# Kernel tuning notes

Measured on AMD Instinct MI355X. Metric: run time of the kernel, lower is better.

Reference implementation:

```python
import jax, jax.numpy as jnp
import numpy as np

D_MODEL = 1024
H = 16
D_K = D_MODEL // H
NEG = -1e9


def setup_inputs() -> dict:
    key = jax.random.key(0)
    ks = jax.random.split(key, 13)
    B, S = 4, 2048
    q = jax.random.normal(ks[0], (B, S, D_MODEL), dtype=jnp.float32)
    k = jax.random.normal(ks[1], (B, S, D_MODEL), dtype=jnp.float32)
    v = jax.random.normal(ks[2], (B, S, D_MODEL), dtype=jnp.float32)
    mask = jax.random.randint(ks[3], (B, 1, S, S), 0, 2, dtype=jnp.int32)
    s = 1.0 / np.sqrt(D_MODEL)
    wq = jax.random.uniform(ks[4], (D_MODEL, D_MODEL), jnp.float32, -s, s)
    bq = jax.random.uniform(ks[5], (D_MODEL,), jnp.float32, -s, s)
    wk = jax.random.uniform(ks[6], (D_MODEL, D_MODEL), jnp.float32, -s, s)
    bk = jax.random.uniform(ks[7], (D_MODEL,), jnp.float32, -s, s)
    wv = jax.random.uniform(ks[8], (D_MODEL, D_MODEL), jnp.float32, -s, s)
    bv = jax.random.uniform(ks[9], (D_MODEL,), jnp.float32, -s, s)
    wo = jax.random.uniform(ks[10], (D_MODEL, D_MODEL), jnp.float32, -s, s)
    bo = jax.random.uniform(ks[11], (D_MODEL,), jnp.float32, -s, s)
    return {"q": q, "k": k, "v": v, "mask": mask,
            "wq": wq, "bq": bq, "wk": wk, "bk": bk,
            "wv": wv, "bv": bv, "wo": wo, "bo": bo}


def reference(q, k, v, mask, wq, bq, wk, bk, wv, bv, wo, bo):
    B, S, _ = q.shape
    # projections (torch Linear: x @ W.T + b)
    query = q @ wq.T + bq
    key_ = k @ wk.T + bk
    value = v @ wv.T + bv
    # [B, S, H, D_K] -> [B, H, S, D_K]
    query = query.reshape(B, S, H, D_K).transpose(0, 2, 1, 3)
    key_ = key_.reshape(B, S, H, D_K).transpose(0, 2, 1, 3)
    value = value.reshape(B, S, H, D_K).transpose(0, 2, 1, 3)
    scores = jnp.einsum('bhqd,bhkd->bhqk', query, key_) / jnp.sqrt(jnp.float32(D_K))
    scores = jnp.where(mask == 0, jnp.float32(NEG), scores)
    attn = jax.nn.softmax(scores, axis=-1)  # dropout p=0 -> identity
    x = jnp.einsum('bhqk,bhkd->bhqd', attn, value)
    x = x.transpose(0, 2, 1, 3).reshape(B, S, D_MODEL)
    return x @ wo.T + bo
```

## Files before the change

kernel.cpp:

```cpp
#include <hip/hip_runtime.h>
#include <stdint.h>
#include <stddef.h>


typedef unsigned short ushort_t;
typedef unsigned long long u64;
typedef __attribute__((ext_vector_type(8))) short short8;
typedef __attribute__((ext_vector_type(4))) float floatx4;
typedef __attribute__((ext_vector_type(4))) unsigned short ushort4v;
typedef __attribute__((ext_vector_type(4))) unsigned int uint4v;

#define QSCALE (0.125f * 1.4426950408889634f)

__device__ __forceinline__ ushort_t f2bf(float f) {
    union { float ff; unsigned int i; } v; v.ff = f;
    unsigned int u = v.i;
    return (ushort_t)((u + 0x7fffu + ((u >> 16) & 1u)) >> 16);
}
__device__ __forceinline__ unsigned int pk2(float a, float b) {
    unsigned int r;
    asm("v_cvt_pk_bf16_f32 %0, %1, %2" : "=v"(r) : "v"(a), "v"(b));
    return r;
}
__device__ __forceinline__ float fexp2(float x) {
#if __has_builtin(__builtin_amdgcn_exp2f)
    return __builtin_amdgcn_exp2f(x);
#else
    return exp2f(x);
#endif
}
__device__ __forceinline__ void g2l16(const void* g, void* l) {
    __builtin_amdgcn_global_load_lds(
        (const __attribute__((address_space(1))) void*)(uintptr_t)g,
        (__attribute__((address_space(3))) void*)(uint32_t)(uintptr_t)l,
        16, 0, 0);
}

__global__ __launch_bounds__(256) void prep(
    const float* __restrict__ wq, const float* __restrict__ wk,
    const float* __restrict__ wv, const float* __restrict__ wo,
    const float* __restrict__ q, const float* __restrict__ k,
    const float* __restrict__ v, const int* __restrict__ mask,
    ushort_t* __restrict__ Wb, ushort_t* __restrict__ Qb,
    ushort_t* __restrict__ Kb, ushort_t* __restrict__ Vb,
    u64* __restrict__ mbits)
{
    const int bx = blockIdx.x, tid = threadIdx.x;
    if (bx < 14336) {
        const float* src; ushort_t* dst; int idx;
        if (bx < 2048) {
            const int seg = bx >> 9;
            src = (seg == 0) ? wq : (seg == 1) ? wk : (seg == 2) ? wv : wo;
            dst = Wb + (size_t)seg * 1024 * 1024;
            idx = (bx & 511) * 256 + tid;
        } else {
            const int b2 = bx - 2048;
            const int z = b2 >> 12;
            src = (z == 0) ? q : (z == 1) ? k : v;
            dst = (z == 0) ? Qb : (z == 1) ? Kb : Vb;
            idx = (b2 & 4095) * 256 + tid;
        }
        const float4 f0 = ((const float4*)src)[idx * 2];
        const float4 f1 = ((const float4*)src)[idx * 2 + 1];
        uint4v c;
        c.x = pk2(f0.x, f0.y); c.y = pk2(f0.z, f0.w);
        c.z = pk2(f1.x, f1.y); c.w = pk2(f1.z, f1.w);
        ((uint4v*)dst)[idx] = c;
    } else {
        const int b3 = bx - 14336;
        const int base = b3 * 4096;
#pragma unroll
        for (int it = 0; it < 16; ++it) {
            const int gid = base + it * 256 + tid;
            const u64 bits = __ballot(mask[gid] != 0);
            if ((tid & 63) == 0) mbits[gid >> 6] = bits;
        }
    }
}

__device__ __forceinline__ void gemm_core(
    const ushort_t* __restrict__ Ain, const ushort_t* __restrict__ W,
    const float* __restrict__ bias, void* __restrict__ Cout,
    float scale, int mode)
{
    constexpr int N = 1024, K = 1024;
    __shared__ alignas(16) ushort_t As[4][128 * 32];
    __shared__ alignas(16) ushort_t Bs[2][128 * 32];

    const int tid  = threadIdx.x;
    const int lane = tid & 63;
    const int w    = tid >> 6;
    const int quad = lane >> 4;
    const int l16  = lane & 15;
    const int wm = w >> 1, wn = w & 1;
    const int bm = blockIdx.x * 128, bn = blockIdx.y * 128;

    const int ar0 = tid >> 2,         acs0 = ((tid & 3) ^ (ar0 & 3)) * 8;
    const int ar1 = (tid + 256) >> 2, acs1 = ((tid & 3) ^ (ar1 & 3)) * 8;
    const ushort_t* Ast0 = Ain + (size_t)(bm + ar0) * K + acs0;
    const ushort_t* Ast1 = Ain + (size_t)(bm + ar1) * K + acs1;
    const ushort_t* Wst0 = W + (size_t)(bn + ar0) * K + acs0;
    const ushort_t* Wst1 = W + (size_t)(bn + ar1) * K + acs1;

    const int ksw = (quad ^ (l16 & 3)) * 8;
    int asoff[4], bsoff[4];
#pragma unroll
    for (int i = 0; i < 4; i++) {
        asoff[i] = (wm * 64 + i * 16 + l16) * 32 + ksw;
        bsoff[i] = (wn * 64 + i * 16 + l16) * 32 + ksw;
    }

    floatx4 acc[4][4] = {};

    g2l16(Wst0,      &Bs[0][tid * 8]);
    g2l16(Wst1,      &Bs[0][(tid + 256) * 8]);
    __builtin_amdgcn_sched_barrier(0);
    g2l16(Ast0,      &As[0][tid * 8]);
    g2l16(Ast1,      &As[0][(tid + 256) * 8]);
    g2l16(Ast0 + 32, &As[1][tid * 8]);
    g2l16(Ast1 + 32, &As[1][(tid + 256) * 8]);
    g2l16(Ast0 + 64, &As[2][tid * 8]);
    g2l16(Ast1 + 64, &As[2][(tid + 256) * 8]);

#define GITER(AS, WS, NW, NA, KW, KA, DO_W, DO_A, TOPW) do {                  \
    asm volatile("s_waitcnt " TOPW);                                          \
    asm volatile("s_waitcnt lgkmcnt(0)");                                     \
    __builtin_amdgcn_sched_barrier(0);                                        \
    __builtin_amdgcn_s_barrier();                                             \
    __builtin_amdgcn_sched_barrier(0);                                        \
    if (DO_W) {                                                               \
        g2l16(Wst0 + (KW), &Bs[NW][tid * 8]);                                 \
        g2l16(Wst1 + (KW), &Bs[NW][(tid + 256) * 8]);                         \
    }                                                                         \
    __builtin_amdgcn_sched_barrier(0);                                        \
    if (DO_A) {                                                               \
        g2l16(Ast0 + (KA), &As[NA][tid * 8]);                                 \
        g2l16(Ast1 + (KA), &As[NA][(tid + 256) * 8]);                         \
    }                                                                         \
    __builtin_amdgcn_sched_barrier(0);                                        \
    {                                                                         \
        short8 af[4], bf[4];                                                  \
        _Pragma("unroll")                                                     \
        for (int i = 0; i < 4; i++) af[i] = *(const short8*)&As[AS][asoff[i]];\
        _Pragma("unroll")                                                     \
        for (int i = 0; i < 4; i++) bf[i] = *(const short8*)&Bs[WS][bsoff[i]];\
        _Pragma("unroll")                                                     \
        for (int mi = 0; mi < 4; mi++)                                        \
        _Pragma("unroll")                                                     \
        for (int ni = 0; ni < 4; ni++)                                        \
            acc[mi][ni] = __builtin_amdgcn_mfma_f32_16x16x32_bf16(            \
                af[mi], bf[ni], acc[mi][ni], 0, 0, 0);                        \
    }                                                                         \
} while (0)

    GITER(0, 0, 1, 3,  32,  96, true, true, "vmcnt(4)");
    GITER(1, 1, 0, 0,  64, 128, true, true, "vmcnt(2)");
    GITER(2, 0, 1, 1,  96, 160, true, true, "vmcnt(2)");
    GITER(3, 1, 0, 2, 128, 192, true, true, "vmcnt(2)");
    for (int j = 1; j < 7; ++j) {
        const int kb = j * 128;
        GITER(0, 0, 1, 3, kb + 32,  kb + 96,  true, true, "vmcnt(2)");
        GITER(1, 1, 0, 0, kb + 64,  kb + 128, true, true, "vmcnt(2)");
        GITER(2, 0, 1, 1, kb + 96,  kb + 160, true, true, "vmcnt(2)");
        GITER(3, 1, 0, 2, kb + 128, kb + 192, true, true, "vmcnt(2)");
    }
    GITER(0, 0, 1, 3, 928, 992, true,  true,  "vmcnt(2)");
    GITER(1, 1, 0, 0, 960, 0,   true,  false, "vmcnt(2)");
    GITER(2, 0, 1, 0, 992, 0,   true,  false, "vmcnt(0)");
    GITER(3, 1, 0, 0, 0,   0,   false, false, "vmcnt(0)");
#undef GITER

#pragma unroll
    for (int ni = 0; ni < 4; ni++) {
        const int n = bn + wn * 64 + ni * 16 + l16;
        const float bv_ = bias[n];
#pragma unroll
        for (int mi = 0; mi < 4; mi++) {
            const int mbase = bm + wm * 64 + mi * 16 + quad * 4;
            if (mode == 2) {
                const int b_ = mbase >> 11, s0 = mbase & 2047;
                const int h = n >> 6, d = n & 63;
                ushort4v pk_;
#pragma unroll
                for (int r = 0; r < 4; r++)
                    pk_[r] = f2bf((acc[mi][ni][r] + bv_) * scale);
                *(ushort4v*)&((ushort_t*)Cout)[
                    (((size_t)(b_ * 16 + h)) * 64 + d) * 2048 + s0] = pk_;
            } else {
#pragma unroll
                for (int r = 0; r < 4; r++) {
                    const int m = mbase + r;
                    const float of = (acc[mi][ni][r] + bv_) * scale;
                    if (mode == 0) {
                        ((float*)Cout)[(size_t)m * N + n] = of;
                    } else {
                        const int b_ = m >> 11, s = m & 2047;
                        const int h = n >> 6, d = n & 63;
                        ((ushort_t*)Cout)[(((size_t)(b_ * 16 + h)) * 2048 + s) * 64 + d]
                            = f2bf(of);
                    }
                }
            }
        }
    }
}

__global__ __launch_bounds__(256, 3) void gemm_qkv(
    const ushort_t* __restrict__ Qb, const ushort_t* __restrict__ Kb,
    const ushort_t* __restrict__ Vb, const ushort_t* __restrict__ Wb,
    const float* __restrict__ bq, const float* __restrict__ bk,
    const float* __restrict__ bv,
    ushort_t* __restrict__ Qp, ushort_t* __restrict__ Kp,
    ushort_t* __restrict__ Vtp)
{
    const int z = blockIdx.z;
    const ushort_t* A = (z == 0) ? Qb : (z == 1) ? Kb : Vb;
    const ushort_t* W = Wb + (size_t)z * 1024 * 1024;
    const float* bi = (z == 0) ? bq : (z == 1) ? bk : bv;
    void* C = (z == 0) ? (void*)Qp : (z == 1) ? (void*)Kp : (void*)Vtp;
    const float sc = (z == 0) ? QSCALE : 1.0f;
    const int mode = (z == 2) ? 2 : 1;
    gemm_core(A, W, bi, C, sc, mode);
}

__global__ __launch_bounds__(256, 3) void gemm_out(
    const ushort_t* __restrict__ X, const ushort_t* __restrict__ W,
    const float* __restrict__ bo, float* __restrict__ out)
{
    gemm_core(X, W, bo, out, 1.0f, 0);
}

__global__ __launch_bounds__(256, 4) void attn(
    const ushort_t* __restrict__ Q,
    const ushort_t* __restrict__ Kk,
    const ushort_t* __restrict__ Vt,
    const u64* __restrict__ mb,
    ushort_t* __restrict__ X)
{
    constexpr int S = 2048;
    __shared__ alignas(16) ushort_t Ks[2][64 * 64];
    __shared__ alignas(16) ushort_t Vs[2][64 * 64];
    __shared__ alignas(16) ushort_t Ps[4][16 * 64];

    const int tid  = threadIdx.x;
    const int lane = tid & 63;
    const int w    = tid >> 6;
    const int quad = lane >> 4;
    const int l16  = lane & 15;
    const int bh = blockIdx.x;
    const int b  = bh >> 4, h = bh & 15;
    const int qbase = blockIdx.y * 64 + w * 16;
    const int qlane = qbase + l16;

    const int r0 = tid >> 3,         cs0 = ((tid & 7) ^ (r0 & 7)) * 8;
    const int r1 = (tid + 256) >> 3, cs1 = ((tid & 7) ^ (r1 & 7)) * 8;

    const ushort_t* Kst0 = &Kk[((size_t)bh * S + r0) * 64 + cs0];
    const ushort_t* Kst1 = &Kk[((size_t)bh * S + r1) * 64 + cs1];
    const ushort_t* Vst0 = &Vt[((size_t)bh * 64 + r0) * S + cs0];
    const ushort_t* Vst1 = &Vt[((size_t)bh * 64 + r1) * S + cs1];

    const int swz = l16 & 7;
    int kvoff[2][4], pfoff[2], pwoff[4];
#pragma unroll
    for (int ks = 0; ks < 2; ks++) {
        pfoff[ks] = l16 * 64 + (((ks * 4 + quad) ^ swz) * 8);
#pragma unroll
        for (int ni = 0; ni < 4; ni++)
            kvoff[ks][ni] = (ni * 16 + l16) * 64 + (((ks * 4 + quad) ^ swz) * 8);
    }
#pragma unroll
    for (int ni = 0; ni < 4; ni++)
        pwoff[ni] = l16 * 64 + (((ni * 2 + (quad >> 1)) ^ swz) * 8) + (quad & 1) * 4;
    ushort_t* Psw = &Ps[w][0];

    short8 qf[2];
#pragma unroll
    for (int ks = 0; ks < 2; ks++)
        qf[ks] = *(const short8*)&Q[((size_t)bh * S + qlane) * 64 + ks * 32 + quad * 8];

    short8 onesv;
#pragma unroll
    for (int i = 0; i < 8; i++) onesv[i] = (short)0x3F80;

    const u64* mrow = mb + ((size_t)b * S + qlane) * 32;

    floatx4 o[4] = {};
    floatx4 lf = {};

    g2l16(Kst0, &Ks[0][tid * 8]);
    g2l16(Kst1, &Ks[0][(tid + 256) * 8]);
    g2l16(Vst0, &Vs[0][tid * 8]);
    g2l16(Vst1, &Vs[0][(tid + 256) * 8]);
    __syncthreads();

    int cur = 0;
    for (int kt = 0; kt < 32; kt++) {
        if (kt < 31) {
            g2l16(Kst0 + (kt + 1) * 4096, &Ks[cur ^ 1][tid * 8]);
            g2l16(Kst1 + (kt + 1) * 4096, &Ks[cur ^ 1][(tid + 256) * 8]);
            g2l16(Vst0 + (kt + 1) * 64,   &Vs[cur ^ 1][tid * 8]);
            g2l16(Vst1 + (kt + 1) * 64,   &Vs[cur ^ 1][(tid + 256) * 8]);
        }
        const ushort_t* Ksc = &Ks[cur][0];
        const ushort_t* Vsc = &Vs[cur][0];

        floatx4 s[4] = {};
        __builtin_amdgcn_s_setprio(1);
#pragma unroll
        for (int ks = 0; ks < 2; ks++)
#pragma unroll
            for (int ni = 0; ni < 4; ni++)
                s[ni] = __builtin_amdgcn_mfma_f32_16x16x32_bf16(
                    *(const short8*)&Ksc[kvoff[ks][ni]], qf[ks], s[ni], 0, 0, 0);
        __builtin_amdgcn_s_setprio(0);

        const u64 mw = mrow[kt];
#pragma unroll
        for (int ni = 0; ni < 4; ni++) {
            const unsigned int t = (unsigned int)(mw >> (ni * 16 + quad * 4));
#pragma unroll
            for (int r = 0; r < 4; r++)
                s[ni][r] = (t & (1u << r)) ? fexp2(s[ni][r]) : 0.f;
        }

#pragma unroll
        for (int ni = 0; ni < 4; ni++) {
            const unsigned int lo = pk2(s[ni][0], s[ni][1]);
            const unsigned int hi = pk2(s[ni][2], s[ni][3]);
            const unsigned long long dv = ((unsigned long long)hi << 32) | lo;
            *(unsigned long long*)&Psw[pwoff[ni]] = dv;
        }

        __builtin_amdgcn_s_setprio(1);
#pragma unroll
        for (int ks = 0; ks < 2; ks++) {
            const short8 pf = *(const short8*)&Psw[pfoff[ks]];
            lf = __builtin_amdgcn_mfma_f32_16x16x32_bf16(onesv, pf, lf, 0, 0, 0);
#pragma unroll
            for (int ni = 0; ni < 4; ni++)
                o[ni] = __builtin_amdgcn_mfma_f32_16x16x32_bf16(
                    *(const short8*)&Vsc[kvoff[ks][ni]], pf, o[ni], 0, 0, 0);
        }
        __builtin_amdgcn_s_setprio(0);
        __syncthreads();
        cur ^= 1;
    }

    const float inv = 1.0f / lf[0];
#pragma unroll
    for (int ni = 0; ni < 4; ni++) {
        ushort4v pk_;
#pragma unroll
        for (int r = 0; r < 4; r++) pk_[r] = f2bf(o[ni][r] * inv);
        *(ushort4v*)&X[((size_t)b * S + qlane) * 1024 + h * 64 + ni * 16 + quad * 4] = pk_;
    }
}

extern "C" void kernel_launch(void* const* d_in, const int* in_sizes, int n_in,
                              void* d_out, int out_size, void* d_ws, size_t ws_size,
                              hipStream_t stream) {
    const float* q    = (const float*)d_in[0];
    const float* k    = (const float*)d_in[1];
    const float* v    = (const float*)d_in[2];
    const int*   mask = (const int*)d_in[3];
    const float* wq   = (const float*)d_in[4];
    const float* bq   = (const float*)d_in[5];
    const float* wk   = (const float*)d_in[6];
    const float* bk   = (const float*)d_in[7];
    const float* wv   = (const float*)d_in[8];
    const float* bv   = (const float*)d_in[9];
    const float* wo   = (const float*)d_in[10];
    const float* bo   = (const float*)d_in[11];

    const size_t MB = 1024 * 1024;
    uint8_t* ws = (uint8_t*)d_ws;
    ushort_t* Wb   = (ushort_t*)(ws);
    u64*      mbits= (u64*)(ws + 8 * MB);
    ushort_t* Qp   = (ushort_t*)(ws + 10 * MB);
    ushort_t* Kp   = (ushort_t*)(ws + 26 * MB);
    ushort_t* Vtp  = (ushort_t*)(ws + 42 * MB);
    ushort_t* Xp   = (ushort_t*)(ws + 58 * MB);
    ushort_t* Qb   = (ushort_t*)(ws + 58 * MB);
    ushort_t* Kb   = (ushort_t*)(ws + 74 * MB);
    ushort_t* Vb   = (ushort_t*)(ws + 90 * MB);

    dim3 blk(256);

    prep<<<dim3(18432), blk, 0, stream>>>(wq, wk, wv, wo, q, k, v, mask,
                                          Wb, Qb, Kb, Vb, mbits);

    gemm_qkv<<<dim3(64, 8, 3), blk, 0, stream>>>(Qb, Kb, Vb, Wb, bq, bk, bv,
                                                 Qp, Kp, Vtp);

    attn<<<dim3(64, 32), blk, 0, stream>>>(Qp, Kp, Vtp, mbits, Xp);

    gemm_out<<<dim3(64, 8), blk, 0, stream>>>(Xp, Wb + 3 * MB, bo, (float*)d_out);
}
```

Measured before the change: 403.5 us.

## Fuse fp32-to-bf16 activation conversion into QKV GEMM A-tile loading

The QKV projection GEMM now reads fp32 q/k/v directly, converts each tile to bf16 in registers and stores it into LDS, so the prep kernel no longer converts and writes bf16 copies of the activations. This removes a full round trip of 3x8M elements through global memory. In exchange the QKV GEMM loses its deeper async global-to-LDS pipeline, uses a simpler double buffer with register staging, and drops its occupancy hint from 3 to 2. Smaller changes also prefetch the mask word one iteration ahead in attention, add MFMA priority hints, and change the LDS swizzle pattern.

```diff
diff --git a/kernel.cpp b/kernel.cpp
--- a/kernel.cpp
+++ b/kernel.cpp
@@ -35,31 +35,30 @@
         (__attribute__((address_space(3))) void*)(uint32_t)(uintptr_t)l,
         16, 0, 0);
 }
+__device__ __forceinline__ void cvt_store(ushort_t* d0, ushort_t* d1,
+        float4 a, float4 b, float4 c, float4 d) {
+    uint4v c0, c1;
+    c0.x = pk2(a.x, a.y); c0.y = pk2(a.z, a.w);
+    c0.z = pk2(b.x, b.y); c0.w = pk2(b.z, b.w);
+    c1.x = pk2(c.x, c.y); c1.y = pk2(c.z, c.w);
+    c1.z = pk2(d.x, d.y); c1.w = pk2(d.z, d.w);
+    *(uint4v*)d0 = c0;
+    *(uint4v*)d1 = c1;
+}
 
 __global__ __launch_bounds__(256) void prep(
     const float* __restrict__ wq, const float* __restrict__ wk,
     const float* __restrict__ wv, const float* __restrict__ wo,
-    const float* __restrict__ q, const float* __restrict__ k,
-    const float* __restrict__ v, const int* __restrict__ mask,
-    ushort_t* __restrict__ Wb, ushort_t* __restrict__ Qb,
-    ushort_t* __restrict__ Kb, ushort_t* __restrict__ Vb,
-    u64* __restrict__ mbits)
+    const int* __restrict__ mask,
+    ushort_t* __restrict__ Wb, u64* __restrict__ mbits)
 {
     const int bx = blockIdx.x, tid = threadIdx.x;
-    if (bx < 14336) {
-        const float* src; ushort_t* dst; int idx;
-        if (bx < 2048) {
-            const int seg = bx >> 9;
-            src = (seg == 0) ? wq : (seg == 1) ? wk : (seg == 2) ? wv : wo;
-            dst = Wb + (size_t)seg * 1024 * 1024;
-            idx = (bx & 511) * 256 + tid;
-        } else {
-            const int b2 = bx - 2048;
-            const int z = b2 >> 12;
-            src = (z == 0) ? q : (z == 1) ? k : v;
-            dst = (z == 0) ? Qb : (z == 1) ? Kb : Vb;
-            idx = (b2 & 4095) * 256 + tid;
-        }
+    if (bx < 2048) {
+        const int seg = bx >> 9;
+        const float* src = (seg == 0) ? wq : (seg == 1) ? wk
+                         : (seg == 2) ? wv : wo;
+        ushort_t* dst = Wb + (size_t)seg * 1024 * 1024;
+        const int idx = (bx & 511) * 256 + tid;
         const float4 f0 = ((const float4*)src)[idx * 2];
         const float4 f1 = ((const float4*)src)[idx * 2 + 1];
         uint4v c;
@@ -67,7 +66,7 @@
         c.z = pk2(f1.x, f1.y); c.w = pk2(f1.z, f1.w);
         ((uint4v*)dst)[idx] = c;
     } else {
-        const int b3 = bx - 14336;
+        const int b3 = bx - 2048;
         const int base = b3 * 4096;
 #pragma unroll
         for (int it = 0; it < 16; ++it) {
@@ -78,13 +77,54 @@
     }
 }
 
-__device__ __forceinline__ void gemm_core(
-    const ushort_t* __restrict__ Ain, const ushort_t* __restrict__ W,
+__device__ __forceinline__ void gemm_epilogue(
+    floatx4 (&acc)[4][4], const float* __restrict__ bias,
+    void* __restrict__ Cout, float scale, int mode,
+    int bm, int bn, int wm, int wn, int quad, int l16)
+{
+    constexpr int N = 1024;
+#pragma unroll
+    for (int ni = 0; ni < 4; ni++) {
+        const int n = bn + wn * 64 + ni * 16 + l16;
+        const float bv_ = bias[n];
+#pragma unroll
+        for (int mi = 0; mi < 4; mi++) {
+            const int mbase = bm + wm * 64 + mi * 16 + quad * 4;
+            if (mode == 2) {
+                const int b_ = mbase >> 11, s0 = mbase & 2047;
+                const int h = n >> 6, d = n & 63;
+                ushort4v pk_;
+#pragma unroll
+                for (int r = 0; r < 4; r++)
+                    pk_[r] = f2bf((acc[mi][ni][r] + bv_) * scale);
+                *(ushort4v*)&((ushort_t*)Cout)[
+                    (((size_t)(b_ * 16 + h)) * 64 + d) * 2048 + s0] = pk_;
+            } else {
+#pragma unroll
+                for (int r = 0; r < 4; r++) {
+                    const int m = mbase + r;
+                    const float of = (acc[mi][ni][r] + bv_) * scale;
+                    if (mode == 0) {
+                        ((float*)Cout)[(size_t)m * N + n] = of;
+                    } else {
+                        const int b_ = m >> 11, s = m & 2047;
+                        const int h = n >> 6, d = n & 63;
+                        ((ushort_t*)Cout)[(((size_t)(b_ * 16 + h)) * 2048 + s) * 64 + d]
+                            = f2bf(of);
+                    }
+                }
+            }
+        }
+    }
+}
+
+__device__ __forceinline__ void gemm_core_f32(
+    const float* __restrict__ Ain, const ushort_t* __restrict__ W,
     const float* __restrict__ bias, void* __restrict__ Cout,
     float scale, int mode)
 {
-    constexpr int N = 1024, K = 1024;
-    __shared__ alignas(16) ushort_t As[4][128 * 32];
+    constexpr int K = 1024;
+    __shared__ alignas(16) ushort_t As[2][128 * 32];
     __shared__ alignas(16) ushort_t Bs[2][128 * 32];
 
     const int tid  = threadIdx.x;
@@ -95,14 +135,97 @@
     const int wm = w >> 1, wn = w & 1;
     const int bm = blockIdx.x * 128, bn = blockIdx.y * 128;
 
-    const int ar0 = tid >> 2,         acs0 = ((tid & 3) ^ (ar0 & 3)) * 8;
-    const int ar1 = (tid + 256) >> 2, acs1 = ((tid & 3) ^ (ar1 & 3)) * 8;
-    const ushort_t* Ast0 = Ain + (size_t)(bm + ar0) * K + acs0;
-    const ushort_t* Ast1 = Ain + (size_t)(bm + ar1) * K + acs1;
-    const ushort_t* Wst0 = W + (size_t)(bn + ar0) * K + acs0;
-    const ushort_t* Wst1 = W + (size_t)(bn + ar1) * K + acs1;
-
-    const int ksw = (quad ^ (l16 & 3)) * 8;
+    const int wrow = tid >> 2;
+    const int wcs  = ((tid & 3) ^ ((tid >> 3) & 3)) * 8;
+    const ushort_t* Wst0 = W + (size_t)(bn + wrow) * K + wcs;
+    const ushort_t* Wst1 = W + (size_t)(bn + wrow + 64) * K + wcs;
+
+    const int arow = tid >> 1, ahalf = tid & 1;
+    const float* Af = Ain + (size_t)(bm + arow) * K + ahalf * 16;
+    const int fa  = (tid >> 2) & 3;
+    const int ac0 = ((2 * ahalf + 0) ^ fa) * 8;
+    const int ac1 = ((2 * ahalf + 1) ^ fa) * 8;
+
+    const int ksw = (quad ^ ((l16 >> 1) & 3)) * 8;
+    int asoff[4], bsoff[4];
+#pragma unroll
+    for (int i = 0; i < 4; i++) {
+        asoff[i] = (wm * 64 + i * 16 + l16) * 32 + ksw;
+        bsoff[i] = (wn * 64 + i * 16 + l16) * 32 + ksw;
+    }
+
+    floatx4 acc[4][4] = {};
+
+    {
+        const float4* ap = (const float4*)Af;
+        const float4 f0 = ap[0], f1 = ap[1], f2 = ap[2], f3 = ap[3];
+        g2l16(Wst0, &Bs[0][tid * 8]);
+        g2l16(Wst1, &Bs[0][(tid + 256) * 8]);
+        cvt_store(&As[0][arow * 32 + ac0], &As[0][arow * 32 + ac1],
+                  f0, f1, f2, f3);
+    }
+    __syncthreads();
+
+    int cur = 0;
+    for (int kt = 0; kt < K; kt += 32) {
+        const int nxt = kt + 32;
+        float4 f0, f1, f2, f3;
+        if (nxt < K) {
+            const float4* ap = (const float4*)(Af + nxt);
+            f0 = ap[0]; f1 = ap[1]; f2 = ap[2]; f3 = ap[3];
+            g2l16(Wst0 + nxt, &Bs[cur ^ 1][tid * 8]);
+            g2l16(Wst1 + nxt, &Bs[cur ^ 1][(tid + 256) * 8]);
+        }
+
+        short8 af[4], bf[4];
+#pragma unroll
+        for (int i = 0; i < 4; i++) af[i] = *(const short8*)&As[cur][asoff[i]];
+#pragma unroll
+        for (int i = 0; i < 4; i++) bf[i] = *(const short8*)&Bs[cur][bsoff[i]];
+        __builtin_amdgcn_s_setprio(1);
+#pragma unroll
+        for (int mi = 0; mi < 4; mi++)
+#pragma unroll
+            for (int ni = 0; ni < 4; ni++)
+                acc[mi][ni] = __builtin_amdgcn_mfma_f32_16x16x32_bf16(
+                    af[mi], bf[ni], acc[mi][ni], 0, 0, 0);
+        __builtin_amdgcn_s_setprio(0);
+
+        if (nxt < K)
+            cvt_store(&As[cur ^ 1][arow * 32 + ac0],
+                      &As[cur ^ 1][arow * 32 + ac1], f0, f1, f2, f3);
+        __syncthreads();
+        cur ^= 1;
+    }
+
+    gemm_epilogue(acc, bias, Cout, scale, mode, bm, bn, wm, wn, quad, l16);
+}
+
+__device__ __forceinline__ void gemm_core_bf16(
+    const ushort_t* __restrict__ Ain, const ushort_t* __restrict__ W,
+    const float* __restrict__ bias, void* __restrict__ Cout,
+    float scale, int mode)
+{
+    constexpr int K = 1024;
+    __shared__ alignas(16) ushort_t As[4][128 * 32];
+    __shared__ alignas(16) ushort_t Bs[2][128 * 32];
+
+    const int tid  = threadIdx.x;
+    const int lane = tid & 63;
+    const int w    = tid >> 6;
+    const int quad = lane >> 4;
+    const int l16  = lane & 15;
+    const int wm = w >> 1, wn = w & 1;
+    const int bm = blockIdx.x * 128, bn = blockIdx.y * 128;
+
+    const int srow = tid >> 2;
+    const int scs  = ((tid & 3) ^ ((tid >> 3) & 3)) * 8;
+    const ushort_t* Ast0 = Ain + (size_t)(bm + srow) * K + scs;
+    const ushort_t* Ast1 = Ain + (size_t)(bm + srow + 64) * K + scs;
+    const ushort_t* Wst0 = W + (size_t)(bn + srow) * K + scs;
+    const ushort_t* Wst1 = W + (size_t)(bn + srow + 64) * K + scs;
+
+    const int ksw = (quad ^ ((l16 >> 1) & 3)) * 8;
     int asoff[4], bsoff[4];
 #pragma unroll
     for (int i = 0; i < 4; i++) {
@@ -144,12 +267,14 @@
         for (int i = 0; i < 4; i++) af[i] = *(const short8*)&As[AS][asoff[i]];\
         _Pragma("unroll")                                                     \
         for (int i = 0; i < 4; i++) bf[i] = *(const short8*)&Bs[WS][bsoff[i]];\
+        __builtin_amdgcn_s_setprio(1);                                        \
         _Pragma("unroll")                                                     \
         for (int mi = 0; mi < 4; mi++)                                        \
         _Pragma("unroll")                                                     \
         for (int ni = 0; ni < 4; ni++)                                        \
             acc[mi][ni] = __builtin_amdgcn_mfma_f32_16x16x32_bf16(            \
                 af[mi], bf[ni], acc[mi][ni], 0, 0, 0);                        \
+        __builtin_amdgcn_s_setprio(0);                                        \
     }                                                                         \
 } while (0)
 
@@ -170,64 +295,32 @@
     GITER(3, 1, 0, 0, 0,   0,   false, false, "vmcnt(0)");
 #undef GITER
 
-#pragma unroll
-    for (int ni = 0; ni < 4; ni++) {
-        const int n = bn + wn * 64 + ni * 16 + l16;
-        const float bv_ = bias[n];
-#pragma unroll
-        for (int mi = 0; mi < 4; mi++) {
-            const int mbase = bm + wm * 64 + mi * 16 + quad * 4;
-            if (mode == 2) {
-                const int b_ = mbase >> 11, s0 = mbase & 2047;
-                const int h = n >> 6, d = n & 63;
-                ushort4v pk_;
-#pragma unroll
-                for (int r = 0; r < 4; r++)
-                    pk_[r] = f2bf((acc[mi][ni][r] + bv_) * scale);
-                *(ushort4v*)&((ushort_t*)Cout)[
-                    (((size_t)(b_ * 16 + h)) * 64 + d) * 2048 + s0] = pk_;
-            } else {
-#pragma unroll
-                for (int r = 0; r < 4; r++) {
-                    const int m = mbase + r;
-                    const float of = (acc[mi][ni][r] + bv_) * scale;
-                    if (mode == 0) {
-                        ((float*)Cout)[(size_t)m * N + n] = of;
-                    } else {
-                        const int b_ = m >> 11, s = m & 2047;
-                        const int h = n >> 6, d = n & 63;
-                        ((ushort_t*)Cout)[(((size_t)(b_ * 16 + h)) * 2048 + s) * 64 + d]
-                            = f2bf(of);
-                    }
-                }
-            }
-        }
-    }
-}
-
-__global__ __launch_bounds__(256, 3) void gemm_qkv(
-    const ushort_t* __restrict__ Qb, const ushort_t* __restrict__ Kb,
-    const ushort_t* __restrict__ Vb, const ushort_t* __restrict__ Wb,
+    gemm_epilogue(acc, bias, Cout, scale, mode, bm, bn, wm, wn, quad, l16);
+}
+
+__global__ __launch_bounds__(256, 2) void gemm_qkv(
+    const float* __restrict__ q, const float* __restrict__ k,
+    const float* __restrict__ v, const ushort_t* __restrict__ Wb,
     const float* __restrict__ bq, const float* __restrict__ bk,
     const float* __restrict__ bv,
     ushort_t* __restrict__ Qp, ushort_t* __restrict__ Kp,
     ushort_t* __restrict__ Vtp)
 {
     const int z = blockIdx.z;
-    const ushort_t* A = (z == 0) ? Qb : (z == 1) ? Kb : Vb;
+    const float* A = (z == 0) ? q : (z == 1) ? k : v;
     const ushort_t* W = Wb + (size_t)z * 1024 * 1024;
     const float* bi = (z == 0) ? bq : (z == 1) ? bk : bv;
     void* C = (z == 0) ? (void*)Qp : (z == 1) ? (void*)Kp : (void*)Vtp;
     const float sc = (z == 0) ? QSCALE : 1.0f;
     const int mode = (z == 2) ? 2 : 1;
-    gemm_core(A, W, bi, C, sc, mode);
+    gemm_core_f32(A, W, bi, C, sc, mode);
 }
 
 __global__ __launch_bounds__(256, 3) void gemm_out(
     const ushort_t* __restrict__ X, const ushort_t* __restrict__ W,
     const float* __restrict__ bo, float* __restrict__ out)
 {
-    gemm_core(X, W, bo, out, 1.0f, 0);
+    gemm_core_bf16(X, W, bo, out, 1.0f, 0);
 }
 
 __global__ __launch_bounds__(256, 4) void attn(
@@ -294,9 +387,12 @@
     g2l16(Vst1, &Vs[0][(tid + 256) * 8]);
     __syncthreads();
 
+    u64 mw = mrow[0];
     int cur = 0;
     for (int kt = 0; kt < 32; kt++) {
+        u64 mw_nxt = 0;
         if (kt < 31) {
+            mw_nxt = mrow[kt + 1];
             g2l16(Kst0 + (kt + 1) * 4096, &Ks[cur ^ 1][tid * 8]);
             g2l16(Kst1 + (kt + 1) * 4096, &Ks[cur ^ 1][(tid + 256) * 8]);
             g2l16(Vst0 + (kt + 1) * 64,   &Vs[cur ^ 1][tid * 8]);
@@ -315,7 +411,6 @@
                     *(const short8*)&Ksc[kvoff[ks][ni]], qf[ks], s[ni], 0, 0, 0);
         __builtin_amdgcn_s_setprio(0);
 
-        const u64 mw = mrow[kt];
 #pragma unroll
         for (int ni = 0; ni < 4; ni++) {
             const unsigned int t = (unsigned int)(mw >> (ni * 16 + quad * 4));
@@ -344,6 +439,7 @@
         }
         __builtin_amdgcn_s_setprio(0);
         __syncthreads();
+        mw = mw_nxt;
         cur ^= 1;
     }
 
@@ -381,16 +477,12 @@
     ushort_t* Kp   = (ushort_t*)(ws + 26 * MB);
     ushort_t* Vtp  = (ushort_t*)(ws + 42 * MB);
     ushort_t* Xp   = (ushort_t*)(ws + 58 * MB);
-    ushort_t* Qb   = (ushort_t*)(ws + 58 * MB);
-    ushort_t* Kb   = (ushort_t*)(ws + 74 * MB);
-    ushort_t* Vb   = (ushort_t*)(ws + 90 * MB);
 
     dim3 blk(256);
 
-    prep<<<dim3(18432), blk, 0, stream>>>(wq, wk, wv, wo, q, k, v, mask,
-                                          Wb, Qb, Kb, Vb, mbits);
-
-    gemm_qkv<<<dim3(64, 8, 3), blk, 0, stream>>>(Qb, Kb, Vb, Wb, bq, bk, bv,
+    prep<<<dim3(6144), blk, 0, stream>>>(wq, wk, wv, wo, mask, Wb, mbits);
+
+    gemm_qkv<<<dim3(64, 8, 3), blk, 0, stream>>>(q, k, v, Wb, bq, bk, bv,
                                                  Qp, Kp, Vtp);
 
     attn<<<dim3(64, 32), blk, 0, stream>>>(Qp, Kp, Vtp, mbits, Xp);
```

Result: slower. 427.0 us (+5.8%).

## Split output projection GEMM along K into two partials plus a reduce kernel

Applied to the files above, without the earlier changes.

Replaces the single output-projection GEMM (512 blocks) with a split-K version that launches 1024 blocks, each covering half of K and writing fp32 partial sums. A separate reduce kernel then adds the two partials and the bias. The aim is more parallelism and occupancy for the last GEMM. The cost is 32 MB of extra fp32 partial writes and reads plus one more kernel launch. The dedicated kernel also uses a three-stage A buffer and raises the occupancy hint to 4.

```diff
diff --git a/kernel.cpp b/kernel.cpp
--- a/kernel.cpp
+++ b/kernel.cpp
@@ -83,7 +83,7 @@
     const float* __restrict__ bias, void* __restrict__ Cout,
     float scale, int mode)
 {
-    constexpr int N = 1024, K = 1024;
+    constexpr int K = 1024;
     __shared__ alignas(16) ushort_t As[4][128 * 32];
     __shared__ alignas(16) ushort_t Bs[2][128 * 32];
 
@@ -191,14 +191,10 @@
                 for (int r = 0; r < 4; r++) {
                     const int m = mbase + r;
                     const float of = (acc[mi][ni][r] + bv_) * scale;
-                    if (mode == 0) {
-                        ((float*)Cout)[(size_t)m * N + n] = of;
-                    } else {
-                        const int b_ = m >> 11, s = m & 2047;
-                        const int h = n >> 6, d = n & 63;
-                        ((ushort_t*)Cout)[(((size_t)(b_ * 16 + h)) * 2048 + s) * 64 + d]
-                            = f2bf(of);
-                    }
+                    const int b_ = m >> 11, s = m & 2047;
+                    const int h = n >> 6, d = n & 63;
+                    ((ushort_t*)Cout)[(((size_t)(b_ * 16 + h)) * 2048 + s) * 64 + d]
+                        = f2bf(of);
                 }
             }
         }
@@ -223,11 +219,130 @@
     gemm_core(A, W, bi, C, sc, mode);
 }
 
-__global__ __launch_bounds__(256, 3) void gemm_out(
-    const ushort_t* __restrict__ X, const ushort_t* __restrict__ W,
-    const float* __restrict__ bo, float* __restrict__ out)
+__global__ __launch_bounds__(256, 4) void gemm_outp(
+    const ushort_t* __restrict__ X, const ushort_t* __restrict__ Wo,
+    float* __restrict__ P0, float* __restrict__ P1)
 {
-    gemm_core(X, W, bo, out, 1.0f, 0);
+    constexpr int K = 1024, N = 1024;
+    __shared__ alignas(16) ushort_t As[3][128 * 32];
+    __shared__ alignas(16) ushort_t Bs[2][128 * 32];
+
+    const int tid  = threadIdx.x;
+    const int lane = tid & 63;
+    const int w    = tid >> 6;
+    const int quad = lane >> 4;
+    const int l16  = lane & 15;
+    const int wm = w >> 1, wn = w & 1;
+    const int bm = blockIdx.x * 128, bn = blockIdx.y * 128;
+    const int kz = blockIdx.z * 512;
+    float* P = blockIdx.z ? P1 : P0;
+
+    const int ar0 = tid >> 2,         acs0 = ((tid & 3) ^ (ar0 & 3)) * 8;
+    const int ar1 = (tid + 256) >> 2, acs1 = ((tid & 3) ^ (ar1 & 3)) * 8;
+    const ushort_t* Ast0 = X + (size_t)(bm + ar0) * K + kz + acs0;
+    const ushort_t* Ast1 = X + (size_t)(bm + ar1) * K + kz + acs1;
+    const ushort_t* Wst0 = Wo + (size_t)(bn + ar0) * K + kz + acs0;
+    const ushort_t* Wst1 = Wo + (size_t)(bn + ar1) * K + kz + acs1;
+
+    const int ksw = (quad ^ (l16 & 3)) * 8;
+    int asoff[4], bsoff[4];
+#pragma unroll
+    for (int i = 0; i < 4; i++) {
+        asoff[i] = (wm * 64 + i * 16 + l16) * 32 + ksw;
+        bsoff[i] = (wn * 64 + i * 16 + l16) * 32 + ksw;
+    }
+
+    floatx4 acc[4][4] = {};
+
+    g2l16(Wst0,      &Bs[0][tid * 8]);
+    g2l16(Wst1,      &Bs[0][(tid + 256) * 8]);
+    __builtin_amdgcn_sched_barrier(0);
+    g2l16(Ast0,      &As[0][tid * 8]);
+    g2l16(Ast1,      &As[0][(tid + 256) * 8]);
+    g2l16(Ast0 + 32, &As[1][tid * 8]);
+    g2l16(Ast1 + 32, &As[1][(tid + 256) * 8]);
+
+#define OITER(AS, WS, NW, NA, KW, KA, DO_W, DO_A, TOPW) do {                  \
+    asm volatile("s_waitcnt " TOPW);                                          \
+    asm volatile("s_waitcnt lgkmcnt(0)");                                     \
+    __builtin_amdgcn_sched_barrier(0);                                        \
+    __builtin_amdgcn_s_barrier();                                             \
+    __builtin_amdgcn_sched_barrier(0);                                        \
+    if (DO_W) {                                                               \
+        g2l16(Wst0 + (KW), &Bs[NW][tid * 8]);                                 \
+        g2l16(Wst1 + (KW), &Bs[NW][(tid + 256) * 8]);                         \
+    }                                                                         \
+    __builtin_amdgcn_sched_barrier(0);                                        \
+    if (DO_A) {                                                               \
+        g2l16(Ast0 + (KA), &As[NA][tid * 8]);                                 \
+        g2l16(Ast1 + (KA), &As[NA][(tid + 256) * 8]);                         \
+    }                                                                         \
+    __builtin_amdgcn_sched_barrier(0);                                        \
+    {                                                                         \
+        short8 af[4], bf[4];                                                  \
+        _Pragma("unroll")                                                     \
+        for (int i = 0; i < 4; i++) af[i] = *(const short8*)&As[AS][asoff[i]];\
+        _Pragma("unroll")                                                     \
+        for (int i = 0; i < 4; i++) bf[i] = *(const short8*)&Bs[WS][bsoff[i]];\
+        _Pragma("unroll")                                                     \
+        for (int mi = 0; mi < 4; mi++)                                        \
+        _Pragma("unroll")                                                     \
+        for (int ni = 0; ni < 4; ni++)                                        \
+            acc[mi][ni] = __builtin_amdgcn_mfma_f32_16x16x32_bf16(            \
+                af[mi], bf[ni], acc[mi][ni], 0, 0, 0);                        \
+    }                                                                         \
+} while (0)
+
+    OITER(0, 0, 1, 2,  32,  64, true, true, "vmcnt(2)");
+    OITER(1, 1, 0, 0,  64,  96, true, true, "vmcnt(2)");
+    OITER(2, 0, 1, 1,  96, 128, true, true, "vmcnt(2)");
+    OITER(0, 1, 0, 2, 128, 160, true, true, "vmcnt(2)");
+    OITER(1, 0, 1, 0, 160, 192, true, true, "vmcnt(2)");
+    OITER(2, 1, 0, 1, 192, 224, true, true, "vmcnt(2)");
+    OITER(0, 0, 1, 2, 224, 256, true, true, "vmcnt(2)");
+    OITER(1, 1, 0, 0, 256, 288, true, true, "vmcnt(2)");
+    OITER(2, 0, 1, 1, 288, 320, true, true, "vmcnt(2)");
+    OITER(0, 1, 0, 2, 320, 352, true, true, "vmcnt(2)");
+    OITER(1, 0, 1, 0, 352, 384, true, true, "vmcnt(2)");
+    OITER(2, 1, 0, 1, 384, 416, true, true, "vmcnt(2)");
+    OITER(0, 0, 1, 2, 416, 448, true, true, "vmcnt(2)");
+    OITER(1, 1, 0, 0, 448, 480, true, true, "vmcnt(2)");
+    OITER(2, 0, 1, 0, 480, 0,   true, false, "vmcnt(2)");
+    OITER(0, 1, 0, 0, 0,   0,   false, false, "vmcnt(0)");
+#undef OITER
+
+#pragma unroll
+    for (int ni = 0; ni < 4; ni++) {
+        const int n = bn + wn * 64 + ni * 16 + l16;
+#pragma unroll
+        for (int mi = 0; mi < 4; mi++) {
+            const int mbase = bm + wm * 64 + mi * 16 + quad * 4;
+#pragma unroll
+            for (int r = 0; r < 4; r++)
+                P[(size_t)(mbase + r) * N + n] = acc[mi][ni][r];
+        }
+    }
+}
+
+__global__ __launch_bounds__(256) void reduce_out(
+    const float* __restrict__ P0, const float* __restrict__ P1,
+    const float* __restrict__ bias, float* __restrict__ out)
+{
+    const int i = blockIdx.x * 256 + threadIdx.x;
+    const int nb = (i * 8) & 1023;
+    const float4 a0 = ((const float4*)P0)[i * 2];
+    const float4 a1 = ((const float4*)P0)[i * 2 + 1];
+    const float4 b0 = ((const float4*)P1)[i * 2];
+    const float4 b1 = ((const float4*)P1)[i * 2 + 1];
+    const float4 c0 = *(const float4*)&bias[nb];
+    const float4 c1 = *(const float4*)&bias[nb + 4];
+    float4 o0, o1;
+    o0.x = a0.x + b0.x + c0.x; o0.y = a0.y + b0.y + c0.y;
+    o0.z = a0.z + b0.z + c0.z; o0.w = a0.w + b0.w + c0.w;
+    o1.x = a1.x + b1.x + c1.x; o1.y = a1.y + b1.y + c1.y;
+    o1.z = a1.z + b1.z + c1.z; o1.w = a1.w + b1.w + c1.w;
+    ((float4*)out)[i * 2]     = o0;
+    ((float4*)out)[i * 2 + 1] = o1;
 }
 
 __global__ __launch_bounds__(256, 4) void attn(
@@ -384,6 +499,8 @@
     ushort_t* Qb   = (ushort_t*)(ws + 58 * MB);
     ushort_t* Kb   = (ushort_t*)(ws + 74 * MB);
     ushort_t* Vb   = (ushort_t*)(ws + 90 * MB);
+    float*    P0   = (float*)(ws + 10 * MB);
+    float*    P1   = (float*)(ws + 74 * MB);
 
     dim3 blk(256);
 
@@ -395,5 +512,7 @@
 
     attn<<<dim3(64, 32), blk, 0, stream>>>(Qp, Kp, Vtp, mbits, Xp);
 
-    gemm_out<<<dim3(64, 8), blk, 0, stream>>>(Xp, Wb + 3 * MB, bo, (float*)d_out);
-}
+    gemm_outp<<<dim3(64, 8, 2), blk, 0, stream>>>(Xp, Wb + 3 * MB, P0, P1);
+
+    reduce_out<<<dim3(4096), blk, 0, stream>>>(P0, P1, bo, (float*)d_out);
+}
```

Measured after the change: 422.7 us. 4.8% more time.
